# Optimization experiments

Hardware: AMD Instinct MI355X
Metric: run time of the kernel (lower is better)

The kernel has to match this reference:

```python
import jax, jax.numpy as jnp
import numpy as np

IN_FEATURES = 8192
OUT_FEATURES = 8192
MAX_STATES = 100
THRESHOLD = MAX_STATES // 2  # 50


def setup_inputs() -> dict:
    key = jax.random.key(0)
    k1, k2 = jax.random.split(key)
    # synapse_states ~ Normal(threshold-5, 3), clamped to [1, max_states]
    states = THRESHOLD - 5.0 + 3.0 * jax.random.normal(k1, (OUT_FEATURES, IN_FEATURES), dtype=jnp.float32)
    states = jnp.clip(states, 1.0, float(MAX_STATES))
    spike_input = (jax.random.uniform(k2, (IN_FEATURES,), dtype=jnp.float32) < 0.2).astype(jnp.float32)
    return {
        'spike_input': spike_input,
        'synapse_states': states,
        'membrane_potential': jnp.zeros((OUT_FEATURES,), dtype=jnp.float32),
        'adaptive_threshold': jnp.full((OUT_FEATURES,), 4.0, dtype=jnp.float32),
        'eligibility_trace': jnp.zeros((OUT_FEATURES, IN_FEATURES), dtype=jnp.float32),
    }


def reference(spike_input, synapse_states, membrane_potential, adaptive_threshold, eligibility_trace):
    # ternary (here effectively binary) weights from synapse states
    w = (synapse_states > float(THRESHOLD)).astype(jnp.float32)          # [O, I]
    x = spike_input                                                       # [I]
    conn_sum = jnp.maximum(jnp.sum(w, axis=1), 5.0)                       # [O]
    current = (w @ x) * (15.0 / jnp.sqrt(conn_sum))                       # [O]
    v_mem = membrane_potential * 0.85 + current                           # leaky integrate
    spikes = (v_mem >= adaptive_threshold).astype(jnp.float32)            # fire
    # eligibility trace update: decay + outer(spikes, x), clamped to [0, 5]
    new_trace = jnp.clip(eligibility_trace * 0.9 + jnp.outer(spikes, x), 0.0, 5.0)
    # adaptive threshold update, clamped to [2, 15]
    new_threshold = jnp.clip(adaptive_threshold + (spikes - 0.1) * 0.1, 2.0, 15.0)
    # soft reset of membrane potential
    new_v_mem = v_mem * (1.0 - spikes) * 0.1
    return spikes, new_v_mem, new_threshold, new_trace
```

## Files before the change

### kernel.cpp

```cpp
#include <hip/hip_runtime.h>

#define IN_F 8192
#define OUT_F 8192

typedef float v4f __attribute__((ext_vector_type(4)));

__global__ __launch_bounds__(256) void snn_fused_kernel(
    const float* __restrict__ x,
    const float* __restrict__ states,
    const float* __restrict__ mp,
    const float* __restrict__ thr,
    const float* __restrict__ trace,
    float* __restrict__ out)
{
    const int o = blockIdx.x;
    const int t = threadIdx.x;

    __shared__ float red_ws[4];
    __shared__ float red_dot[4];

    const float mp_o  = mp[o];
    const float thr_o = thr[o];

    const v4f* __restrict__ x4  = (const v4f*)x;
    const v4f* __restrict__ s4  = (const v4f*)(states + (size_t)o * IN_F);
    const v4f* __restrict__ tr4 = (const v4f*)(trace  + (size_t)o * IN_F);

    v4f xr[8], tr[8];
    float wsum = 0.0f, dot = 0.0f;
#pragma unroll
    for (int k = 0; k < 8; ++k) {
        const int idx = t + (k << 8);
        xr[k] = x4[idx];
        tr[k] = __builtin_nontemporal_load(&tr4[idx]);
        const v4f sv = __builtin_nontemporal_load(&s4[idx]);
        const float w0 = (sv[0] > 50.0f) ? 1.0f : 0.0f;
        const float w1 = (sv[1] > 50.0f) ? 1.0f : 0.0f;
        const float w2 = (sv[2] > 50.0f) ? 1.0f : 0.0f;
        const float w3 = (sv[3] > 50.0f) ? 1.0f : 0.0f;
        wsum += (w0 + w1) + (w2 + w3);
        dot  += (w0 * xr[k][0] + w1 * xr[k][1]) + (w2 * xr[k][2] + w3 * xr[k][3]);
    }

#pragma unroll
    for (int off = 32; off > 0; off >>= 1) {
        wsum += __shfl_down(wsum, off);
        dot  += __shfl_down(dot,  off);
    }
    const int wave = t >> 6;
    if ((t & 63) == 0) { red_ws[wave] = wsum; red_dot[wave] = dot; }
    __syncthreads();

    const float ws = (red_ws[0] + red_ws[1]) + (red_ws[2] + red_ws[3]);
    const float dt = (red_dot[0] + red_dot[1]) + (red_dot[2] + red_dot[3]);
    const float conn    = fmaxf(ws, 5.0f);
    const float current = dt * (15.0f / sqrtf(conn));
    const float v       = mp_o * 0.85f + current;
    const float spike   = (v >= thr_o) ? 1.0f : 0.0f;

    if (t == 0) {
        out[o]             = spike;
        out[OUT_F + o]     = v * (1.0f - spike) * 0.1f;
        out[2 * OUT_F + o] = fminf(fmaxf(thr_o + (spike - 0.1f) * 0.1f, 2.0f), 15.0f);
    }

    v4f* __restrict__ ot4 = (v4f*)(out + 3 * OUT_F + (size_t)o * IN_F);
#pragma unroll
    for (int k = 0; k < 8; ++k) {
        const int idx = t + (k << 8);
        v4f r;
        r[0] = fminf(fmaxf(tr[k][0] * 0.9f + spike * xr[k][0], 0.0f), 5.0f);
        r[1] = fminf(fmaxf(tr[k][1] * 0.9f + spike * xr[k][1], 0.0f), 5.0f);
        r[2] = fminf(fmaxf(tr[k][2] * 0.9f + spike * xr[k][2], 0.0f), 5.0f);
        r[3] = fminf(fmaxf(tr[k][3] * 0.9f + spike * xr[k][3], 0.0f), 5.0f);
        __builtin_nontemporal_store(r, &ot4[idx]);
    }
}

extern "C" void kernel_launch(void* const* d_in, const int* in_sizes, int n_in,
                              void* d_out, int out_size, void* d_ws, size_t ws_size,
                              hipStream_t stream) {
    const float* x      = (const float*)d_in[0];
    const float* states = (const float*)d_in[1];
    const float* mp     = (const float*)d_in[2];
    const float* thr    = (const float*)d_in[3];
    const float* trace  = (const float*)d_in[4];
    float* out = (float*)d_out;

    snn_fused_kernel<<<OUT_F, 256, 0, stream>>>(x, states, mp, thr, trace, out);
}
```

Baseline: 559.6 us.

## Assign one wavefront per output row and drop block-level reduction

Each 64-lane wavefront now handles a whole output row, so a 256-thread block covers four rows. The cross-wave shared-memory reduction and __syncthreads go away, and reductions use xor shuffles. The trace load moves after the spike is computed and is no longer held in registers across the reduction, which lowers register pressure but serialises the trace read behind the states read for each wave. The kernel is memory bound at roughly 800MB of traffic, so the main risk is reduced memory-level parallelism per wave.

```diff
diff --git a/kernel.cpp b/kernel.cpp
--- a/kernel.cpp
+++ b/kernel.cpp
@@ -5,7 +5,7 @@
 
 typedef float v4f __attribute__((ext_vector_type(4)));
 
-__global__ __launch_bounds__(256) void snn_fused_kernel(
+__global__ __launch_bounds__(256) void snn_wave_kernel(
     const float* __restrict__ x,
     const float* __restrict__ states,
     const float* __restrict__ mp,
@@ -13,66 +13,57 @@
     const float* __restrict__ trace,
     float* __restrict__ out)
 {
-    const int o = blockIdx.x;
-    const int t = threadIdx.x;
-
-    __shared__ float red_ws[4];
-    __shared__ float red_dot[4];
+    const int lane = threadIdx.x & 63;
+    const int o    = (blockIdx.x << 2) + (threadIdx.x >> 6);
 
     const float mp_o  = mp[o];
     const float thr_o = thr[o];
 
-    const v4f* __restrict__ x4  = (const v4f*)x;
-    const v4f* __restrict__ s4  = (const v4f*)(states + (size_t)o * IN_F);
-    const v4f* __restrict__ tr4 = (const v4f*)(trace  + (size_t)o * IN_F);
+    const v4f* __restrict__ x4 = (const v4f*)x;
+    const v4f* __restrict__ s4 = (const v4f*)(states + (size_t)o * IN_F);
 
-    v4f xr[8], tr[8];
     float wsum = 0.0f, dot = 0.0f;
 #pragma unroll
-    for (int k = 0; k < 8; ++k) {
-        const int idx = t + (k << 8);
-        xr[k] = x4[idx];
-        tr[k] = __builtin_nontemporal_load(&tr4[idx]);
+    for (int k = 0; k < 32; ++k) {
+        const int idx = lane + (k << 6);
         const v4f sv = __builtin_nontemporal_load(&s4[idx]);
+        const v4f xv = x4[idx];
         const float w0 = (sv[0] > 50.0f) ? 1.0f : 0.0f;
         const float w1 = (sv[1] > 50.0f) ? 1.0f : 0.0f;
         const float w2 = (sv[2] > 50.0f) ? 1.0f : 0.0f;
         const float w3 = (sv[3] > 50.0f) ? 1.0f : 0.0f;
         wsum += (w0 + w1) + (w2 + w3);
-        dot  += (w0 * xr[k][0] + w1 * xr[k][1]) + (w2 * xr[k][2] + w3 * xr[k][3]);
+        dot  += (w0 * xv[0] + w1 * xv[1]) + (w2 * xv[2] + w3 * xv[3]);
     }
 
 #pragma unroll
     for (int off = 32; off > 0; off >>= 1) {
-        wsum += __shfl_down(wsum, off);
-        dot  += __shfl_down(dot,  off);
+        wsum += __shfl_xor(wsum, off);
+        dot  += __shfl_xor(dot,  off);
     }
-    const int wave = t >> 6;
-    if ((t & 63) == 0) { red_ws[wave] = wsum; red_dot[wave] = dot; }
-    __syncthreads();
 
-    const float ws = (red_ws[0] + red_ws[1]) + (red_ws[2] + red_ws[3]);
-    const float dt = (red_dot[0] + red_dot[1]) + (red_dot[2] + red_dot[3]);
-    const float conn    = fmaxf(ws, 5.0f);
-    const float current = dt * (15.0f / sqrtf(conn));
-    const float v       = mp_o * 0.85f + current;
+    const float conn    = fmaxf(wsum, 5.0f);
+    const float v       = mp_o * 0.85f + dot * (15.0f / sqrtf(conn));
     const float spike   = (v >= thr_o) ? 1.0f : 0.0f;
 
-    if (t == 0) {
+    if (lane == 0) {
         out[o]             = spike;
         out[OUT_F + o]     = v * (1.0f - spike) * 0.1f;
         out[2 * OUT_F + o] = fminf(fmaxf(thr_o + (spike - 0.1f) * 0.1f, 2.0f), 15.0f);
     }
 
-    v4f* __restrict__ ot4 = (v4f*)(out + 3 * OUT_F + (size_t)o * IN_F);
-#pragma unroll
-    for (int k = 0; k < 8; ++k) {
-        const int idx = t + (k << 8);
+    const v4f* __restrict__ tr4 = (const v4f*)(trace + (size_t)o * IN_F);
+    v4f* __restrict__ ot4       = (v4f*)(out + 3 * OUT_F + (size_t)o * IN_F);
+#pragma unroll 8
+    for (int k = 0; k < 32; ++k) {
+        const int idx = lane + (k << 6);
+        const v4f tv = __builtin_nontemporal_load(&tr4[idx]);
+        const v4f xv = x4[idx];
         v4f r;
-        r[0] = fminf(fmaxf(tr[k][0] * 0.9f + spike * xr[k][0], 0.0f), 5.0f);
-        r[1] = fminf(fmaxf(tr[k][1] * 0.9f + spike * xr[k][1], 0.0f), 5.0f);
-        r[2] = fminf(fmaxf(tr[k][2] * 0.9f + spike * xr[k][2], 0.0f), 5.0f);
-        r[3] = fminf(fmaxf(tr[k][3] * 0.9f + spike * xr[k][3], 0.0f), 5.0f);
+        r[0] = fminf(fmaxf(tv[0] * 0.9f + spike * xv[0], 0.0f), 5.0f);
+        r[1] = fminf(fmaxf(tv[1] * 0.9f + spike * xv[1], 0.0f), 5.0f);
+        r[2] = fminf(fmaxf(tv[2] * 0.9f + spike * xv[2], 0.0f), 5.0f);
+        r[3] = fminf(fmaxf(tv[3] * 0.9f + spike * xv[3], 0.0f), 5.0f);
         __builtin_nontemporal_store(r, &ot4[idx]);
     }
 }
@@ -87,5 +78,5 @@
     const float* trace  = (const float*)d_in[4];
     float* out = (float*)d_out;
 
-    snn_fused_kernel<<<OUT_F, 256, 0, stream>>>(x, states, mp, thr, trace, out);
+    snn_wave_kernel<<<OUT_F / 4, 256, 0, stream>>>(x, states, mp, thr, trace, out);
 }
```

Result: slower. 571.4 us (+2.1%).

## Split fused SNN kernel into reduction kernel and separate trace-update kernel

Applied to the files above, without the earlier changes.

Splits the single fused kernel into two launches. The first reads the states matrix and computes spikes, membrane potential and threshold. The second reads the trace plus the spikes and writes the updated trace, using two blocks per row. This drops the per-thread trace and x register arrays that were held across the block barrier, which should cut register pressure and raise occupancy. The cost is an extra kernel launch and re-reading x, and the trace traffic can no longer overlap with the states reduction inside one kernel.

```diff
diff --git a/kernel.cpp b/kernel.cpp
--- a/kernel.cpp
+++ b/kernel.cpp
@@ -5,12 +5,11 @@
 
 typedef float v4f __attribute__((ext_vector_type(4)));
 
-__global__ __launch_bounds__(256) void snn_fused_kernel(
+__global__ __launch_bounds__(256) void snn_reduce_kernel(
     const float* __restrict__ x,
     const float* __restrict__ states,
     const float* __restrict__ mp,
     const float* __restrict__ thr,
-    const float* __restrict__ trace,
     float* __restrict__ out)
 {
     const int o = blockIdx.x;
@@ -19,27 +18,21 @@
     __shared__ float red_ws[4];
     __shared__ float red_dot[4];
 
-    const float mp_o  = mp[o];
-    const float thr_o = thr[o];
+    const v4f* __restrict__ x4 = (const v4f*)x;
+    const v4f* __restrict__ s4 = (const v4f*)(states + (size_t)o * IN_F);
 
-    const v4f* __restrict__ x4  = (const v4f*)x;
-    const v4f* __restrict__ s4  = (const v4f*)(states + (size_t)o * IN_F);
-    const v4f* __restrict__ tr4 = (const v4f*)(trace  + (size_t)o * IN_F);
-
-    v4f xr[8], tr[8];
     float wsum = 0.0f, dot = 0.0f;
 #pragma unroll
     for (int k = 0; k < 8; ++k) {
         const int idx = t + (k << 8);
-        xr[k] = x4[idx];
-        tr[k] = __builtin_nontemporal_load(&tr4[idx]);
         const v4f sv = __builtin_nontemporal_load(&s4[idx]);
+        const v4f xv = x4[idx];
         const float w0 = (sv[0] > 50.0f) ? 1.0f : 0.0f;
         const float w1 = (sv[1] > 50.0f) ? 1.0f : 0.0f;
         const float w2 = (sv[2] > 50.0f) ? 1.0f : 0.0f;
         const float w3 = (sv[3] > 50.0f) ? 1.0f : 0.0f;
         wsum += (w0 + w1) + (w2 + w3);
-        dot  += (w0 * xr[k][0] + w1 * xr[k][1]) + (w2 * xr[k][2] + w3 * xr[k][3]);
+        dot  += (w0 * xv[0] + w1 * xv[1]) + (w2 * xv[2] + w3 * xv[3]);
     }
 
 #pragma unroll
@@ -51,28 +44,46 @@
     if ((t & 63) == 0) { red_ws[wave] = wsum; red_dot[wave] = dot; }
     __syncthreads();
 
-    const float ws = (red_ws[0] + red_ws[1]) + (red_ws[2] + red_ws[3]);
-    const float dt = (red_dot[0] + red_dot[1]) + (red_dot[2] + red_dot[3]);
-    const float conn    = fmaxf(ws, 5.0f);
-    const float current = dt * (15.0f / sqrtf(conn));
-    const float v       = mp_o * 0.85f + current;
-    const float spike   = (v >= thr_o) ? 1.0f : 0.0f;
-
     if (t == 0) {
+        const float ws = (red_ws[0] + red_ws[1]) + (red_ws[2] + red_ws[3]);
+        const float dt = (red_dot[0] + red_dot[1]) + (red_dot[2] + red_dot[3]);
+        const float conn  = fmaxf(ws, 5.0f);
+        const float v     = mp[o] * 0.85f + dt * (15.0f / sqrtf(conn));
+        const float th    = thr[o];
+        const float spike = (v >= th) ? 1.0f : 0.0f;
         out[o]             = spike;
         out[OUT_F + o]     = v * (1.0f - spike) * 0.1f;
-        out[2 * OUT_F + o] = fminf(fmaxf(thr_o + (spike - 0.1f) * 0.1f, 2.0f), 15.0f);
+        out[2 * OUT_F + o] = fminf(fmaxf(th + (spike - 0.1f) * 0.1f, 2.0f), 15.0f);
     }
+}
 
-    v4f* __restrict__ ot4 = (v4f*)(out + 3 * OUT_F + (size_t)o * IN_F);
+__global__ __launch_bounds__(256) void snn_trace_kernel(
+    const float* __restrict__ x,
+    const float* __restrict__ trace,
+    const float* __restrict__ spikes,
+    float* __restrict__ out_trace)
+{
+    const int t    = threadIdx.x;
+    const int row  = blockIdx.x >> 1;
+    const int half = blockIdx.x & 1;
+
+    const float spike = spikes[row];
+
+    const v4f* __restrict__ x4  = (const v4f*)x;
+    const v4f* __restrict__ tr4 = (const v4f*)(trace + (size_t)row * IN_F);
+    v4f* __restrict__ ot4       = (v4f*)(out_trace + (size_t)row * IN_F);
+
+    const int base = (half << 10) + t;
 #pragma unroll
-    for (int k = 0; k < 8; ++k) {
-        const int idx = t + (k << 8);
+    for (int k = 0; k < 4; ++k) {
+        const int idx = base + (k << 8);
+        const v4f tv = __builtin_nontemporal_load(&tr4[idx]);
+        const v4f xv = x4[idx];
         v4f r;
-        r[0] = fminf(fmaxf(tr[k][0] * 0.9f + spike * xr[k][0], 0.0f), 5.0f);
-        r[1] = fminf(fmaxf(tr[k][1] * 0.9f + spike * xr[k][1], 0.0f), 5.0f);
-        r[2] = fminf(fmaxf(tr[k][2] * 0.9f + spike * xr[k][2], 0.0f), 5.0f);
-        r[3] = fminf(fmaxf(tr[k][3] * 0.9f + spike * xr[k][3], 0.0f), 5.0f);
+        r[0] = fminf(fmaxf(tv[0] * 0.9f + spike * xv[0], 0.0f), 5.0f);
+        r[1] = fminf(fmaxf(tv[1] * 0.9f + spike * xv[1], 0.0f), 5.0f);
+        r[2] = fminf(fmaxf(tv[2] * 0.9f + spike * xv[2], 0.0f), 5.0f);
+        r[3] = fminf(fmaxf(tv[3] * 0.9f + spike * xv[3], 0.0f), 5.0f);
         __builtin_nontemporal_store(r, &ot4[idx]);
     }
 }
@@ -87,5 +98,6 @@
     const float* trace  = (const float*)d_in[4];
     float* out = (float*)d_out;
 
-    snn_fused_kernel<<<OUT_F, 256, 0, stream>>>(x, states, mp, thr, trace, out);
+    snn_reduce_kernel<<<OUT_F, 256, 0, stream>>>(x, states, mp, thr, out);
+    snn_trace_kernel<<<OUT_F * 2, 256, 0, stream>>>(x, trace, out, out + 3 * OUT_F);
 }
```

Measured after the change: 564.2 us. About the same (+0.8%).
